# Kernel optimization log

Hardware: AMD Instinct MI355X
Metric: run time of the kernel (lower is better)

The kernel has to match this reference:

```python
import jax, jax.numpy as jnp
import numpy as np

DT = 0.1
THRESH = 0.01


def setup_inputs() -> dict:
    key = jax.random.key(0)
    ks = jax.random.split(key, 4)
    B, C, H, W = 4, 64, 128, 128
    field = jax.random.normal(ks[0], (B, C, H, W), dtype=jnp.float32)
    # depthwise 3x3 conv weight [C,1,3,3], fan_in = 9
    dw = jax.random.normal(ks[1], (C, 1, 3, 3), dtype=jnp.float32) * (1.0 / 3.0)
    db = jnp.zeros((C,), jnp.float32)
    # 1x1 convs as matrices: w1 [2C, C], w2 [C, 2C]
    w1 = jax.random.normal(ks[2], (2 * C, C), dtype=jnp.float32) * (1.0 / np.sqrt(C))
    b1 = jnp.zeros((2 * C,), jnp.float32)
    w2 = jax.random.normal(ks[3], (C, 2 * C), dtype=jnp.float32) * (1.0 / np.sqrt(2 * C))
    b2 = jnp.zeros((C,), jnp.float32)
    dcoeff = jnp.ones((1,), jnp.float32) * 0.1  # diffusion_coeff init
    return {"field": field, "dw": dw, "db": db, "w1": w1, "b1": b1,
            "w2": w2, "b2": b2, "dcoeff": dcoeff, "max_steps": 50}


def _dynamics(f, dw, db, w1, b1, w2, b2, dcoeff):
    C = f.shape[1]
    diff = jax.lax.conv_general_dilated(
        f, dw, window_strides=(1, 1), padding="SAME",
        feature_group_count=C,
        dimension_numbers=("NCHW", "OIHW", "NCHW")) + db[None, :, None, None]
    h = jax.nn.gelu(jnp.einsum("bchw,oc->bohw", f, w1) + b1[None, :, None, None],
                    approximate=False)
    react = jnp.einsum("bchw,oc->bohw", h, w2) + b2[None, :, None, None]
    return dcoeff[0] * diff + react


def reference(field, dw, db, w1, b1, w2, b2, dcoeff, max_steps):
    def step(carry, _):
        f, done, steps = carry
        deriv = _dynamics(f, dw, db, w1, b1, w2, b2, dcoeff)
        new_f = f + DT * deriv
        change = jnp.mean(jnp.abs(new_f - f))
        f2 = jnp.where(done, f, new_f)          # freeze field once converged
        steps2 = steps + jnp.where(done, 0, 1)  # steps_taken is adaptive
        done2 = done | (change < THRESH)
        return (f2, done2, steps2), None

    init = (field, jnp.asarray(False), jnp.asarray(0, jnp.int32))
    (final_field, _, steps), _ = jax.lax.scan(step, init, None, length=max_steps)
    return final_field, steps
```

## Files before the change

kernel.cpp:

```cpp
#include <hip/hip_runtime.h>
#include <math.h>

#define BATCH 4
#define CCH   64
#define HDIM  128
#define WDIM  128
#define HW    (HDIM * WDIM)
#define NELEM (BATCH * CCH * HW)
#define OCH   128
#define NSTEPS 50
#define NBLK  1024
#define DT 0.1f
#define THRESH 0.01f

typedef short bf16x8 __attribute__((ext_vector_type(8)));
typedef float f32x4  __attribute__((ext_vector_type(4)));

struct Ctl {
    int done;
    int steps;
};

__global__ void init_kernel(Ctl* ctl) {
    ctl->done = 0;
    ctl->steps = 0;
}

__device__ __forceinline__ short f2bf(float x) {
    unsigned u = __float_as_uint(x);
    unsigned r = u + 0x7fff + ((u >> 16) & 1);
    return (short)(r >> 16);
}

__device__ __forceinline__ int pk(float a, float b) {
    return (f2bf(a) & 0xffff) | (((int)f2bf(b)) << 16);
}

__global__ void prep_kernel(const float* __restrict__ w1,
                            const float* __restrict__ w2,
                            short* __restrict__ w1b, short* __restrict__ w2b) {
    int i = blockIdx.x * blockDim.x + threadIdx.x;
    if (i < OCH * CCH) {
        w1b[i] = f2bf(w1[i]);
        w2b[i] = f2bf(w2[i]);
    }
}

__device__ __forceinline__ float gelu_fast(float x) {
    float u  = x * 0.70710678118654752f;
    float au = fabsf(u);
    float t  = __builtin_amdgcn_rcpf(fmaf(0.3275911f, au, 1.0f));
    float p  = fmaf(1.061405429f, t, -1.453152027f);
    p = fmaf(p, t, 1.421413741f);
    p = fmaf(p, t, -0.284496736f);
    p = fmaf(p, t, 0.254829592f);
    p = p * t;
    float ex = __expf(-au * au);
    float e  = fmaf(-p, ex, 1.0f);
    float er = copysignf(e, x);
    return 0.5f * x * (1.0f + er);
}

__global__ __launch_bounds__(256, 4) void step_kernel(
    const float* __restrict__ fin, float* __restrict__ fout,
    const float* __restrict__ dw, const float* __restrict__ db,
    const short* __restrict__ w1b, const float* __restrict__ b1,
    const short* __restrict__ w2b, const float* __restrict__ b2,
    const float* __restrict__ dcoeff, const Ctl* __restrict__ ctl,
    double* __restrict__ psum)
{
    if (ctl->done) return;

    const int tid  = threadIdx.x;
    const int lane = tid & 63;
    const int w    = tid >> 6;
    const int quad = (lane >> 4);
    const int lp   = lane & 15;
    const int blk  = blockIdx.x;
    const int xcd  = blk & 7;
    const int idx  = blk >> 3;
    const int y    = xcd * 16 + (idx & 15);
    const int b    = (idx >> 4) & 3;
    const int seg  = idx >> 6;
    const int px0  = seg * 64;

    __shared__ int4  sBf4[64 * 8];
    __shared__ int4  sH4 [64 * 16];
    __shared__ float sDw[CCH * 9];
    __shared__ float sDb[CCH];
    __shared__ float wred[4];
    short* sBf = (short*)sBf4;
    short* sH  = (short*)sH4;

    for (int i = tid; i < CCH * 9; i += 256) sDw[i] = dw[i];
    if (tid < CCH) sDb[tid] = db[tid];

    bf16x8 a1[2][2];
    #pragma unroll
    for (int mt = 0; mt < 2; ++mt)
        #pragma unroll
        for (int kk = 0; kk < 2; ++kk)
            a1[mt][kk] = *(const bf16x8*)(w1b + (w * 32 + mt * 16 + lp) * CCH
                                          + kk * 32 + quad * 8);
    f32x4 b1v[2];
    #pragma unroll
    for (int mt = 0; mt < 2; ++mt)
        b1v[mt] = *(const f32x4*)(b1 + w * 32 + mt * 16 + quad * 4);
    f32x4 b2v = *(const f32x4*)(b2 + w * 16 + quad * 4);

    {
        const int base = b * CCH * HW + y * WDIM + px0 + lane;
        float f[16];
        #pragma unroll
        for (int i = 0; i < 16; ++i)
            f[i] = fin[base + (w * 16 + i) * HW];
        int4 v0, v1;
        v0.x = pk(f[0], f[1]);  v0.y = pk(f[2], f[3]);
        v0.z = pk(f[4], f[5]);  v0.w = pk(f[6], f[7]);
        v1.x = pk(f[8], f[9]);  v1.y = pk(f[10], f[11]);
        v1.z = pk(f[12], f[13]); v1.w = pk(f[14], f[15]);
        int g0 = (w * 2)     ^ (lane & 7);
        int g1 = (w * 2 + 1) ^ (lane & 7);
        sBf4[lane * 8 + g0] = v0;
        sBf4[lane * 8 + g1] = v1;
    }
    __syncthreads();

    f32x4 acc1[2][4];
    #pragma unroll
    for (int mt = 0; mt < 2; ++mt)
        #pragma unroll
        for (int nt = 0; nt < 4; ++nt)
            acc1[mt][nt] = (f32x4)0.0f;

    #pragma unroll
    for (int kk = 0; kk < 2; ++kk) {
        #pragma unroll
        for (int nt = 0; nt < 4; ++nt) {
            int px = nt * 16 + lp;
            int g  = kk * 4 + quad;
            bf16x8 bfrag = *(const bf16x8*)(sBf + px * 64 + (g ^ (px & 7)) * 8);
            #pragma unroll
            for (int mt = 0; mt < 2; ++mt)
                acc1[mt][nt] = __builtin_amdgcn_mfma_f32_16x16x32_bf16(
                    a1[mt][kk], bfrag, acc1[mt][nt], 0, 0, 0);
        }
    }

    #pragma unroll
    for (int mt = 0; mt < 2; ++mt) {
        #pragma unroll
        for (int nt = 0; nt < 4; ++nt) {
            int px = nt * 16 + lp;
            float h0 = gelu_fast(acc1[mt][nt][0] + b1v[mt][0]);
            float h1 = gelu_fast(acc1[mt][nt][1] + b1v[mt][1]);
            float h2 = gelu_fast(acc1[mt][nt][2] + b1v[mt][2]);
            float h3 = gelu_fast(acc1[mt][nt][3] + b1v[mt][3]);
            int o0  = w * 32 + mt * 16 + quad * 4;
            int g   = o0 >> 3;
            int sub = o0 & 7;
            int gp  = (g & 8) | ((g ^ (px & 7)) & 7);
            int2 hv; hv.x = pk(h0, h1); hv.y = pk(h2, h3);
            *(int2*)(sH + px * 128 + gp * 8 + sub) = hv;
        }
    }
    __syncthreads();

    bf16x8 a2[4];
    #pragma unroll
    for (int kk = 0; kk < 4; ++kk)
        a2[kk] = *(const bf16x8*)(w2b + (w * 16 + lp) * OCH + kk * 32 + quad * 8);

    f32x4 acc2[4];
    #pragma unroll
    for (int nt = 0; nt < 4; ++nt) acc2[nt] = (f32x4)0.0f;

    #pragma unroll
    for (int kk = 0; kk < 4; ++kk) {
        #pragma unroll
        for (int nt = 0; nt < 4; ++nt) {
            int px = nt * 16 + lp;
            int g  = kk * 4 + quad;
            int gp = (g & 8) | ((g ^ (px & 7)) & 7);
            bf16x8 hfrag = *(const bf16x8*)(sH + px * 128 + gp * 8);
            acc2[nt] = __builtin_amdgcn_mfma_f32_16x16x32_bf16(
                a2[kk], hfrag, acc2[nt], 0, 0, 0);
        }
    }

    const float dc = dcoeff[0];
    const bool ym = (y > 0), yp = (y < HDIM - 1);
    float csum = 0.0f;

    #pragma unroll
    for (int r = 0; r < 4; ++r) {
        const int c = w * 16 + quad * 4 + r;
        const float* wk = sDw + c * 9;
        float k0 = wk[0], k1 = wk[1], k2 = wk[2];
        float k3 = wk[3], k4 = wk[4], k5 = wk[5];
        float k6 = wk[6], k7 = wk[7], k8 = wk[8];
        float dbc = sDb[c];
        #pragma unroll
        for (int nt = 0; nt < 4; ++nt) {
            const int px = nt * 16 + lp;
            const int x  = px0 + px;
            const bool xm = (x > 0), xp = (x < WDIM - 1);
            const float* rc = fin + b * CCH * HW + c * HW + y * WDIM + x;

            float a0 = (ym && xm) ? rc[-WDIM - 1] : 0.0f;
            float a1v = ym        ? rc[-WDIM]     : 0.0f;
            float a2v = (ym && xp) ? rc[-WDIM + 1] : 0.0f;
            float m0 = xm ? rc[-1] : 0.0f;
            float m1 = rc[0];
            float m2 = xp ? rc[1]  : 0.0f;
            float p0 = (yp && xm) ? rc[WDIM - 1] : 0.0f;
            float p1 = yp         ? rc[WDIM]     : 0.0f;
            float p2 = (yp && xp) ? rc[WDIM + 1] : 0.0f;

            float d = dbc;
            d += k0 * a0 + k1 * a1v + k2 * a2v;
            d += k3 * m0 + k4 * m1  + k5 * m2;
            d += k6 * p0 + k7 * p1  + k8 * p2;

            float react = acc2[nt][r] + b2v[r];
            float nf = m1 + DT * (dc * d + react);
            fout[b * CCH * HW + c * HW + y * WDIM + x] = nf;
            csum += fabsf(nf - m1);
        }
    }

    float v = csum;
    #pragma unroll
    for (int off = 32; off > 0; off >>= 1) v += __shfl_down(v, off, 64);
    if (lane == 0) wred[w] = v;
    __syncthreads();
    if (tid == 0) {
        psum[blk] = (double)wred[0] + (double)wred[1]
                  + (double)wred[2] + (double)wred[3];
    }
}

__global__ __launch_bounds__(256) void finalize_kernel(
    Ctl* __restrict__ ctl, const double* __restrict__ psum)
{
    if (ctl->done) return;
    __shared__ double sd[256];
    int t = threadIdx.x;
    sd[t] = psum[t] + psum[t + 256] + psum[t + 512] + psum[t + 768];
    __syncthreads();
    for (int off = 128; off > 0; off >>= 1) {
        if (t < off) sd[t] += sd[t + off];
        __syncthreads();
    }
    if (t == 0) {
        ctl->steps += 1;
        float change = (float)(sd[0] * (1.0 / (double)NELEM));
        if (change < THRESH) ctl->done = 1;
    }
}

__global__ void output_kernel(const float* __restrict__ bufA,
                              float* __restrict__ out,
                              const Ctl* __restrict__ ctl)
{
    int i = blockIdx.x * blockDim.x + threadIdx.x;
    bool fromA = (((ctl->steps - 1) & 1) == 0);
    if (i < NELEM && fromA) out[i] = bufA[i];
    if (i == 0) out[NELEM] = (float)ctl->steps;
}

extern "C" void kernel_launch(void* const* d_in, const int* in_sizes, int n_in,
                              void* d_out, int out_size, void* d_ws, size_t ws_size,
                              hipStream_t stream)
{
    const float* field  = (const float*)d_in[0];
    const float* dw     = (const float*)d_in[1];
    const float* db     = (const float*)d_in[2];
    const float* w1     = (const float*)d_in[3];
    const float* b1     = (const float*)d_in[4];
    const float* w2     = (const float*)d_in[5];
    const float* b2     = (const float*)d_in[6];
    const float* dcoeff = (const float*)d_in[7];

    float* out = (float*)d_out;

    char* ws = (char*)d_ws;
    float*  bufA = (float*)ws;
    Ctl*    ctl  = (Ctl*)(ws + (size_t)NELEM * 4);
    short*  w1b  = (short*)(ws + (size_t)NELEM * 4 + 256);
    short*  w2b  = (short*)(ws + (size_t)NELEM * 4 + 256 + 16384);
    double* psum = (double*)(ws + (size_t)NELEM * 4 + 256 + 32768);

    init_kernel<<<1, 1, 0, stream>>>(ctl);
    prep_kernel<<<(OCH * CCH + 255) / 256, 256, 0, stream>>>(w1, w2, w1b, w2b);

    float* bufs[2] = { bufA, out };
    const float* fin = field;
    for (int s = 1; s <= NSTEPS; ++s) {
        float* fout = bufs[(s - 1) & 1];
        step_kernel<<<NBLK, 256, 0, stream>>>(
            fin, fout, dw, db, w1b, b1, w2b, b2, dcoeff, ctl, psum);
        finalize_kernel<<<1, 256, 0, stream>>>(ctl, psum);
        fin = fout;
    }

    output_kernel<<<(NELEM + 255) / 256, 256, 0, stream>>>(bufA, out, ctl);
}
```

Measured before the change: 1.178 ms.

## Stage depthwise-stencil halo rows into LDS as packed bf16 and compute early

The 3x3 depthwise stencil no longer does nine scattered global loads per output. The block now stages the row above, its own row and the row below, plus left and right seam columns, into shared memory as channel-pair-packed bf16. It computes the diffusion term before the MFMA stages, and the H buffer reuses the same LDS region. This removes redundant global and cache traffic and separates the stencil from the epilogue. In exchange it adds LDS footprint, an extra barrier, and bf16 rounding of the neighbour values in the diffusion term.

```diff
diff --git a/kernel.cpp b/kernel.cpp
--- a/kernel.cpp
+++ b/kernel.cpp
@@ -35,6 +35,9 @@
 __device__ __forceinline__ int pk(float a, float b) {
     return (f2bf(a) & 0xffff) | (((int)f2bf(b)) << 16);
 }
+
+__device__ __forceinline__ float bf_lo(int v) { return __int_as_float(v << 16); }
+__device__ __forceinline__ float bf_hi(int v) { return __int_as_float(v & 0xffff0000); }
 
 __global__ void prep_kernel(const float* __restrict__ w1,
                             const float* __restrict__ w2,
@@ -83,14 +86,16 @@
     const int b    = (idx >> 4) & 3;
     const int seg  = idx >> 6;
     const int px0  = seg * 64;
-
-    __shared__ int4  sBf4[64 * 8];
-    __shared__ int4  sH4 [64 * 16];
+    const int fbase = b * CCH * HW + y * WDIM + px0;
+
+    __shared__ int4 sBf4[64 * 8];
+    __shared__ __align__(16) int uni[3 * 64 * 33];
+    __shared__ int   sSeamD[3 * 2 * 33 + 8];
     __shared__ float sDw[CCH * 9];
     __shared__ float sDb[CCH];
     __shared__ float wred[4];
     short* sBf = (short*)sBf4;
-    short* sH  = (short*)sH4;
+    short* sH  = (short*)uni;
 
     for (int i = tid; i < CCH * 9; i += 256) sDw[i] = dw[i];
     if (tid < CCH) sDb[tid] = db[tid];
@@ -102,6 +107,10 @@
         for (int kk = 0; kk < 2; ++kk)
             a1[mt][kk] = *(const bf16x8*)(w1b + (w * 32 + mt * 16 + lp) * CCH
                                           + kk * 32 + quad * 8);
+    bf16x8 a2[4];
+    #pragma unroll
+    for (int kk = 0; kk < 4; ++kk)
+        a2[kk] = *(const bf16x8*)(w2b + (w * 16 + lp) * OCH + kk * 32 + quad * 8);
     f32x4 b1v[2];
     #pragma unroll
     for (int mt = 0; mt < 2; ++mt)
@@ -109,22 +118,111 @@
     f32x4 b2v = *(const f32x4*)(b2 + w * 16 + quad * 4);
 
     {
-        const int base = b * CCH * HW + y * WDIM + px0 + lane;
         float f[16];
         #pragma unroll
         for (int i = 0; i < 16; ++i)
-            f[i] = fin[base + (w * 16 + i) * HW];
+            f[i] = fin[fbase + (w * 16 + i) * HW + lane];
         int4 v0, v1;
-        v0.x = pk(f[0], f[1]);  v0.y = pk(f[2], f[3]);
-        v0.z = pk(f[4], f[5]);  v0.w = pk(f[6], f[7]);
-        v1.x = pk(f[8], f[9]);  v1.y = pk(f[10], f[11]);
+        v0.x = pk(f[0], f[1]);   v0.y = pk(f[2], f[3]);
+        v0.z = pk(f[4], f[5]);   v0.w = pk(f[6], f[7]);
+        v1.x = pk(f[8], f[9]);   v1.y = pk(f[10], f[11]);
         v1.z = pk(f[12], f[13]); v1.w = pk(f[14], f[15]);
         int g0 = (w * 2)     ^ (lane & 7);
         int g1 = (w * 2 + 1) ^ (lane & 7);
         sBf4[lane * 8 + g0] = v0;
         sBf4[lane * 8 + g1] = v1;
-    }
-    __syncthreads();
+        uni[(1 * 64 + lane) * 33 + (w * 8 + 0)] = v0.x;
+        uni[(1 * 64 + lane) * 33 + (w * 8 + 1)] = v0.y;
+        uni[(1 * 64 + lane) * 33 + (w * 8 + 2)] = v0.z;
+        uni[(1 * 64 + lane) * 33 + (w * 8 + 3)] = v0.w;
+        uni[(1 * 64 + lane) * 33 + (w * 8 + 4)] = v1.x;
+        uni[(1 * 64 + lane) * 33 + (w * 8 + 5)] = v1.y;
+        uni[(1 * 64 + lane) * 33 + (w * 8 + 6)] = v1.z;
+        uni[(1 * 64 + lane) * 33 + (w * 8 + 7)] = v1.w;
+    }
+
+    {
+        const int dy = tid >> 7;
+        const int jj = (tid >> 2) & 31;
+        const int q  = tid & 3;
+        const int gy = y + (dy ? 1 : -1);
+        float c0[16], c1[16];
+        if (gy >= 0 && gy < HDIM) {
+            const float* s0 = fin + b * CCH * HW + (2 * jj) * HW + gy * WDIM + px0 + q * 16;
+            const float* s1 = s0 + HW;
+            #pragma unroll
+            for (int k = 0; k < 4; ++k) {
+                float4 u0 = ((const float4*)s0)[k];
+                float4 u1 = ((const float4*)s1)[k];
+                c0[k*4+0] = u0.x; c0[k*4+1] = u0.y; c0[k*4+2] = u0.z; c0[k*4+3] = u0.w;
+                c1[k*4+0] = u1.x; c1[k*4+1] = u1.y; c1[k*4+2] = u1.z; c1[k*4+3] = u1.w;
+            }
+        } else {
+            #pragma unroll
+            for (int k = 0; k < 16; ++k) { c0[k] = 0.0f; c1[k] = 0.0f; }
+        }
+        const int row = dy * 2;
+        #pragma unroll
+        for (int p = 0; p < 16; ++p)
+            uni[(row * 64 + q * 16 + p) * 33 + jj] = pk(c0[p], c1[p]);
+    }
+
+    if (tid < 192) {
+        const int row  = tid >> 6;
+        const int side = (tid >> 5) & 1;
+        const int jj   = tid & 31;
+        const int gy   = y - 1 + row;
+        const int gx   = px0 + (side ? 64 : -1);
+        float v0 = 0.0f, v1 = 0.0f;
+        if (gy >= 0 && gy < HDIM && gx >= 0 && gx < WDIM) {
+            v0 = fin[b * CCH * HW + (2 * jj) * HW + gy * WDIM + gx];
+            v1 = fin[b * CCH * HW + (2 * jj + 1) * HW + gy * WDIM + gx];
+        }
+        sSeamD[(row * 2 + side) * 33 + jj] = pk(v0, v1);
+    }
+
+    __syncthreads();
+
+    const float dc = dcoeff[0];
+    float m1v[4][4];
+    float dacc[4][4];
+
+    #pragma unroll
+    for (int pr = 0; pr < 2; ++pr) {
+        const int c0 = w * 16 + quad * 4 + 2 * pr;
+        const int jj = w * 8 + quad * 2 + pr;
+        const float* wk0 = sDw + c0 * 9;
+        const float* wk1 = sDw + (c0 + 1) * 9;
+        const float db0 = sDb[c0], db1 = sDb[c0 + 1];
+        #pragma unroll
+        for (int nt = 0; nt < 4; ++nt) {
+            const int p = nt * 16 + lp;
+            float m1a = fin[fbase + c0 * HW + p];
+            float m1b = fin[fbase + (c0 + 1) * HW + p];
+            float d0 = db0 + wk0[4] * m1a;
+            float d1 = db1 + wk1[4] * m1b;
+            #pragma unroll
+            for (int dy = 0; dy < 3; ++dy) {
+                #pragma unroll
+                for (int dx = -1; dx <= 1; ++dx) {
+                    if (dy == 1 && dx == 0) continue;
+                    const int pp = p + dx;
+                    const int* src = ((unsigned)pp < 64u)
+                        ? &uni[(dy * 64 + pp) * 33 + jj]
+                        : &sSeamD[(dy * 2 + (dx > 0)) * 33 + jj];
+                    int v = *src;
+                    float wa = wk0[dy * 3 + dx + 1];
+                    float wb = wk1[dy * 3 + dx + 1];
+                    d0 = fmaf(wa, bf_lo(v), d0);
+                    d1 = fmaf(wb, bf_hi(v), d1);
+                }
+            }
+            m1v[nt][2 * pr]     = m1a;
+            m1v[nt][2 * pr + 1] = m1b;
+            dacc[nt][2 * pr]     = dc * d0;
+            dacc[nt][2 * pr + 1] = dc * d1;
+        }
+    }
 
     f32x4 acc1[2][4];
     #pragma unroll
@@ -146,6 +244,8 @@
                     a1[mt][kk], bfrag, acc1[mt][nt], 0, 0, 0);
         }
     }
+
+    __syncthreads();
 
     #pragma unroll
     for (int mt = 0; mt < 2; ++mt) {
@@ -166,11 +266,6 @@
     }
     __syncthreads();
 
-    bf16x8 a2[4];
-    #pragma unroll
-    for (int kk = 0; kk < 4; ++kk)
-        a2[kk] = *(const bf16x8*)(w2b + (w * 16 + lp) * OCH + kk * 32 + quad * 8);
-
     f32x4 acc2[4];
     #pragma unroll
     for (int nt = 0; nt < 4; ++nt) acc2[nt] = (f32x4)0.0f;
@@ -188,43 +283,16 @@
         }
     }
 
-    const float dc = dcoeff[0];
-    const bool ym = (y > 0), yp = (y < HDIM - 1);
     float csum = 0.0f;
-
     #pragma unroll
     for (int r = 0; r < 4; ++r) {
         const int c = w * 16 + quad * 4 + r;
-        const float* wk = sDw + c * 9;
-        float k0 = wk[0], k1 = wk[1], k2 = wk[2];
-        float k3 = wk[3], k4 = wk[4], k5 = wk[5];
-        float k6 = wk[6], k7 = wk[7], k8 = wk[8];
-        float dbc = sDb[c];
-        #pragma unroll
-        for (int nt = 0; nt < 4; ++nt) {
-            const int px = nt * 16 + lp;
-            const int x  = px0 + px;
-            const bool xm = (x > 0), xp = (x < WDIM - 1);
-            const float* rc = fin + b * CCH * HW + c * HW + y * WDIM + x;
-
-            float a0 = (ym && xm) ? rc[-WDIM - 1] : 0.0f;
-            float a1v = ym        ? rc[-WDIM]     : 0.0f;
-            float a2v = (ym && xp) ? rc[-WDIM + 1] : 0.0f;
-            float m0 = xm ? rc[-1] : 0.0f;
-            float m1 = rc[0];
-            float m2 = xp ? rc[1]  : 0.0f;
-            float p0 = (yp && xm) ? rc[WDIM - 1] : 0.0f;
-            float p1 = yp         ? rc[WDIM]     : 0.0f;
-            float p2 = (yp && xp) ? rc[WDIM + 1] : 0.0f;
-
-            float d = dbc;
-            d += k0 * a0 + k1 * a1v + k2 * a2v;
-            d += k3 * m0 + k4 * m1  + k5 * m2;
-            d += k6 * p0 + k7 * p1  + k8 * p2;
-
-            float react = acc2[nt][r] + b2v[r];
-            float nf = m1 + DT * (dc * d + react);
-            fout[b * CCH * HW + c * HW + y * WDIM + x] = nf;
+        #pragma unroll
+        for (int nt = 0; nt < 4; ++nt) {
+            const int p = nt * 16 + lp;
+            float m1 = m1v[nt][r];
+            float nf = m1 + DT * (dacc[nt][r] + acc2[nt][r] + b2v[r]);
+            fout[fbase + c * HW + p] = nf;
             csum += fabsf(nf - m1);
         }
     }
```

Result: slower. 2.127 ms (+80.6%).

## Restructure stencil epilogue to lane-per-pixel with shuffles and LDS-transposed reaction

Applied to the files above, without the earlier changes.

The depthwise 3x3 stencil previously did nine scattered global loads per output in the MFMA accumulator layout. It now has each lane own one pixel across 16 channels. The lane reuses its already-loaded center values, loads the rows above and below once, and gets horizontal neighbours via cross-lane shuffles, with the segment edges staged in a small LDS seam buffer. The MFMA reaction output is transposed through LDS into that layout, which adds a barrier and rounds the reaction term to bf16 before the update, so accuracy may drop slightly.

```diff
diff --git a/kernel.cpp b/kernel.cpp
--- a/kernel.cpp
+++ b/kernel.cpp
@@ -35,6 +35,9 @@
 __device__ __forceinline__ int pk(float a, float b) {
     return (f2bf(a) & 0xffff) | (((int)f2bf(b)) << 16);
 }
+
+__device__ __forceinline__ float bf_lo(int v) { return __int_as_float(v << 16); }
+__device__ __forceinline__ float bf_hi(int v) { return __int_as_float(v & 0xffff0000); }
 
 __global__ void prep_kernel(const float* __restrict__ w1,
                             const float* __restrict__ w2,
@@ -83,17 +86,36 @@
     const int b    = (idx >> 4) & 3;
     const int seg  = idx >> 6;
     const int px0  = seg * 64;
+    const int fbase = b * CCH * HW + y * WDIM + px0;
 
     __shared__ int4  sBf4[64 * 8];
     __shared__ int4  sH4 [64 * 16];
+    __shared__ float sSeam[384];
     __shared__ float sDw[CCH * 9];
     __shared__ float sDb[CCH];
     __shared__ float wred[4];
     short* sBf = (short*)sBf4;
     short* sH  = (short*)sH4;
+    int*   sRi = (int*)sBf4;
 
     for (int i = tid; i < CCH * 9; i += 256) sDw[i] = dw[i];
     if (tid < CCH) sDb[tid] = db[tid];
+
+    if (tid < 192) {
+        #pragma unroll
+        for (int k = 0; k < 2; ++k) {
+            int e    = tid * 2 + k;
+            int row  = e >> 7;
+            int side = (e >> 6) & 1;
+            int ch   = e & 63;
+            int gy   = y - 1 + row;
+            int gx   = px0 + (side ? 64 : -1);
+            float v  = 0.0f;
+            if (gy >= 0 && gy < HDIM && gx >= 0 && gx < WDIM)
+                v = fin[b * CCH * HW + ch * HW + gy * WDIM + gx];
+            sSeam[e] = v;
+        }
+    }
 
     bf16x8 a1[2][2];
     #pragma unroll
@@ -108,16 +130,15 @@
         b1v[mt] = *(const f32x4*)(b1 + w * 32 + mt * 16 + quad * 4);
     f32x4 b2v = *(const f32x4*)(b2 + w * 16 + quad * 4);
 
+    float f[16];
     {
-        const int base = b * CCH * HW + y * WDIM + px0 + lane;
-        float f[16];
         #pragma unroll
         for (int i = 0; i < 16; ++i)
-            f[i] = fin[base + (w * 16 + i) * HW];
+            f[i] = fin[fbase + (w * 16 + i) * HW + lane];
         int4 v0, v1;
-        v0.x = pk(f[0], f[1]);  v0.y = pk(f[2], f[3]);
-        v0.z = pk(f[4], f[5]);  v0.w = pk(f[6], f[7]);
-        v1.x = pk(f[8], f[9]);  v1.y = pk(f[10], f[11]);
+        v0.x = pk(f[0], f[1]);   v0.y = pk(f[2], f[3]);
+        v0.z = pk(f[4], f[5]);   v0.w = pk(f[6], f[7]);
+        v1.x = pk(f[8], f[9]);   v1.y = pk(f[10], f[11]);
         v1.z = pk(f[12], f[13]); v1.w = pk(f[14], f[15]);
         int g0 = (w * 2)     ^ (lane & 7);
         int g1 = (w * 2 + 1) ^ (lane & 7);
@@ -188,45 +209,68 @@
         }
     }
 
+    float hm[16], hp[16];
+    {
+        const float* fb = fin + fbase + lane;
+        if (y > 0) {
+            #pragma unroll
+            for (int i = 0; i < 16; ++i) hm[i] = fb[(w * 16 + i) * HW - WDIM];
+        } else {
+            #pragma unroll
+            for (int i = 0; i < 16; ++i) hm[i] = 0.0f;
+        }
+        if (y < HDIM - 1) {
+            #pragma unroll
+            for (int i = 0; i < 16; ++i) hp[i] = fb[(w * 16 + i) * HW + WDIM];
+        } else {
+            #pragma unroll
+            for (int i = 0; i < 16; ++i) hp[i] = 0.0f;
+        }
+    }
+
+    #pragma unroll
+    for (int nt = 0; nt < 4; ++nt) {
+        int px = nt * 16 + lp;
+        sRi[(w * 8 + quad * 2 + 0) * 64 + px]
+            = pk(acc2[nt][0] + b2v[0], acc2[nt][1] + b2v[1]);
+        sRi[(w * 8 + quad * 2 + 1) * 64 + px]
+            = pk(acc2[nt][2] + b2v[2], acc2[nt][3] + b2v[3]);
+    }
+    __syncthreads();
+
+    float react[16];
+    #pragma unroll
+    for (int ii = 0; ii < 8; ++ii) {
+        int v = sRi[(w * 8 + ii) * 64 + lane];
+        react[2 * ii]     = bf_lo(v);
+        react[2 * ii + 1] = bf_hi(v);
+    }
+
     const float dc = dcoeff[0];
-    const bool ym = (y > 0), yp = (y < HDIM - 1);
     float csum = 0.0f;
 
     #pragma unroll
-    for (int r = 0; r < 4; ++r) {
-        const int c = w * 16 + quad * 4 + r;
+    for (int i = 0; i < 16; ++i) {
+        const int c = w * 16 + i;
         const float* wk = sDw + c * 9;
-        float k0 = wk[0], k1 = wk[1], k2 = wk[2];
-        float k3 = wk[3], k4 = wk[4], k5 = wk[5];
-        float k6 = wk[6], k7 = wk[7], k8 = wk[8];
-        float dbc = sDb[c];
-        #pragma unroll
-        for (int nt = 0; nt < 4; ++nt) {
-            const int px = nt * 16 + lp;
-            const int x  = px0 + px;
-            const bool xm = (x > 0), xp = (x < WDIM - 1);
-            const float* rc = fin + b * CCH * HW + c * HW + y * WDIM + x;
-
-            float a0 = (ym && xm) ? rc[-WDIM - 1] : 0.0f;
-            float a1v = ym        ? rc[-WDIM]     : 0.0f;
-            float a2v = (ym && xp) ? rc[-WDIM + 1] : 0.0f;
-            float m0 = xm ? rc[-1] : 0.0f;
-            float m1 = rc[0];
-            float m2 = xp ? rc[1]  : 0.0f;
-            float p0 = (yp && xm) ? rc[WDIM - 1] : 0.0f;
-            float p1 = yp         ? rc[WDIM]     : 0.0f;
-            float p2 = (yp && xp) ? rc[WDIM + 1] : 0.0f;
-
-            float d = dbc;
-            d += k0 * a0 + k1 * a1v + k2 * a2v;
-            d += k3 * m0 + k4 * m1  + k5 * m2;
-            d += k6 * p0 + k7 * p1  + k8 * p2;
-
-            float react = acc2[nt][r] + b2v[r];
-            float nf = m1 + DT * (dc * d + react);
-            fout[b * CCH * HW + c * HW + y * WDIM + x] = nf;
-            csum += fabsf(nf - m1);
-        }
+        float vm = hm[i], vc = f[i], vp = hp[i];
+        float lm = __shfl_up(vm, 1),  lc = __shfl_up(vc, 1),  lq = __shfl_up(vp, 1);
+        float rm = __shfl_down(vm, 1), rc = __shfl_down(vc, 1), rq = __shfl_down(vp, 1);
+        lm = (lane == 0)  ? sSeam[0 * 128 + 0 + c]   : lm;
+        lc = (lane == 0)  ? sSeam[1 * 128 + 0 + c]   : lc;
+        lq = (lane == 0)  ? sSeam[2 * 128 + 0 + c]   : lq;
+        rm = (lane == 63) ? sSeam[0 * 128 + 64 + c]  : rm;
+        rc = (lane == 63) ? sSeam[1 * 128 + 64 + c]  : rc;
+        rq = (lane == 63) ? sSeam[2 * 128 + 64 + c]  : rq;
+
+        float d = sDb[c];
+        d = fmaf(wk[0], lm, d); d = fmaf(wk[1], vm, d); d = fmaf(wk[2], rm, d);
+        d = fmaf(wk[3], lc, d); d = fmaf(wk[4], vc, d); d = fmaf(wk[5], rc, d);
+        d = fmaf(wk[6], lq, d); d = fmaf(wk[7], vp, d); d = fmaf(wk[8], rq, d);
+
+        float nf = vc + DT * (dc * d + react[i]);
+        fout[fbase + c * HW + lane] = nf;
+        csum += fabsf(nf - vc);
     }
 
     float v = csum;
```

New measurement: 1.234 ms. 4.7% more time.
